# Optimization experiments

Measured on AMD Instinct MI355X. Metric: run time of the kernel, lower is better.

Reference implementation:

```python
import jax, jax.numpy as jnp
import numpy as np

T = 4096      # tokens (batch*seq)
D = 1024      # hidden_size
F = 4096      # intermediate_size
E = 8         # num_local_experts


def setup_inputs() -> dict:
    key = jax.random.key(0)
    ks = jax.random.split(key, 6)
    scale_in = 1.0 / np.sqrt(D)
    scale_f = 1.0 / np.sqrt(F)
    return {
        "x": jax.random.normal(ks[0], (T, D), jnp.float32),
        "gate_w": jax.random.normal(ks[1], (E, D), jnp.float32) * scale_in,
        "gate_b": jnp.zeros((E,), jnp.float32),
        "w1": jax.random.normal(ks[2], (E, F, D), jnp.float32) * scale_in,
        "w3": jax.random.normal(ks[3], (E, F, D), jnp.float32) * scale_in,
        "w2": jax.random.normal(ks[4], (E, D, F), jnp.float32) * scale_f,
        "top_k": 2,
    }


def reference(x, gate_w, gate_b, w1, w3, w2, top_k):
    # --- routing: gate linear -> softmax -> top-k, renormalized ---
    logits = x @ gate_w.T + gate_b                     # [T, E]
    probs = jax.nn.softmax(logits, axis=-1)            # [T, E]
    topk_p, topk_i = jax.lax.top_k(probs, top_k)       # [T, k]
    topk_p = topk_p / jnp.sum(topk_p, axis=-1, keepdims=True)
    # dense combine weights [T, E]: zeros except selected experts
    cw = jnp.zeros((x.shape[0], gate_w.shape[0]), x.dtype)
    cw = cw.at[jnp.arange(x.shape[0])[:, None], topk_i].set(topk_p)
    # --- experts: SwiGLU FFN, computed densely per expert, masked combine ---
    h1 = jnp.einsum('td,efd->etf', x, w1)              # [E, T, F]
    h3 = jnp.einsum('td,efd->etf', x, w3)              # [E, T, F]
    act = jax.nn.silu(h1) * h3                         # [E, T, F]
    expert_out = jnp.einsum('etf,edf->etd', act, w2)   # [E, T, D]
    out = jnp.einsum('etd,te->td', expert_out, cw)     # [T, D]
    return out
```

## Files before the change

kernel.cpp:

```cpp
#include <hip/hip_runtime.h>
#include <hip/hip_bf16.h>

#define T_TOK 4096
#define DIM   1024
#define FDIM  4096
#define NEXP  8
#define BM    128
#define BN    128
#define BK    32

typedef __attribute__((ext_vector_type(8))) short bf16x8_t;
typedef __attribute__((ext_vector_type(4))) float f32x4_t;

#define GLD16(gp, lp) __builtin_amdgcn_global_load_lds( \
    (const __attribute__((address_space(1))) unsigned int*)(gp), \
    (__attribute__((address_space(3))) unsigned int*)(lp), 16, 0, 0)

__device__ __forceinline__ unsigned short f2bf(float f) {
    union { __hip_bfloat16 h; unsigned short u; } c;
    c.h = __float2bfloat16(f);
    return c.u;
}
__device__ __forceinline__ uint4 pack8(const float4& a, const float4& b) {
    union { unsigned short s[8]; uint4 v; } u;
    u.s[0] = f2bf(a.x); u.s[1] = f2bf(a.y); u.s[2] = f2bf(a.z); u.s[3] = f2bf(a.w);
    u.s[4] = f2bf(b.x); u.s[5] = f2bf(b.y); u.s[6] = f2bf(b.z); u.s[7] = f2bf(b.w);
    return u.v;
}

__global__ __launch_bounds__(256) void convert_kernel(
    const float* __restrict__ src, unsigned short* __restrict__ dst, int n8)
{
    int i = blockIdx.x * 256 + threadIdx.x;
    if (i < n8) {
        const float4* s = reinterpret_cast<const float4*>(src) + (size_t)i * 2;
        float4 a = s[0], b = s[1];
        reinterpret_cast<uint4*>(dst)[i] = pack8(a, b);
    }
}

__global__ __launch_bounds__(256) void gate_kernel(
    const float* __restrict__ x, const float* __restrict__ gw,
    const float* __restrict__ gb, int* __restrict__ cnt,
    int* __restrict__ toklist, float* __restrict__ wlist)
{
    const int lane = threadIdx.x & 63;
    const int wv   = threadIdx.x >> 6;
    const int t    = blockIdx.x * 4 + wv;
    const float* xr = x + (size_t)t * DIM;

    float4 xv[4];
#pragma unroll
    for (int c = 0; c < 4; ++c)
        xv[c] = *reinterpret_cast<const float4*>(xr + c * 256 + lane * 4);

    float logit[NEXP];
#pragma unroll
    for (int e = 0; e < NEXP; ++e) {
        const float* gr = gw + e * DIM;
        float s = 0.f;
#pragma unroll
        for (int c = 0; c < 4; ++c) {
            float4 g = *reinterpret_cast<const float4*>(gr + c * 256 + lane * 4);
            s += xv[c].x * g.x + xv[c].y * g.y + xv[c].z * g.z + xv[c].w * g.w;
        }
#pragma unroll
        for (int o = 32; o > 0; o >>= 1) s += __shfl_xor(s, o, 64);
        logit[e] = s + gb[e];
    }

    if (lane == 0) {
        int i1 = 0;
#pragma unroll
        for (int e = 1; e < NEXP; ++e) if (logit[e] > logit[i1]) i1 = e;
        int i2 = (i1 == 0) ? 1 : 0;
#pragma unroll
        for (int e = 0; e < NEXP; ++e)
            if (e != i1 && e != i2 && logit[e] > logit[i2]) i2 = e;
        float eb = expf(logit[i2] - logit[i1]);
        float wA = 1.f / (1.f + eb);
        float wB = eb / (1.f + eb);
        int p = atomicAdd(&cnt[i1], 1);
        toklist[i1 * T_TOK + p] = t; wlist[i1 * T_TOK + p] = wA;
        p = atomicAdd(&cnt[i2], 1);
        toklist[i2 * T_TOK + p] = t; wlist[i2 * T_TOK + p] = wB;
    }
}

__global__ void offsets_kernel(const int* __restrict__ cnt, int* __restrict__ offs)
{
    if (threadIdx.x == 0) {
        int o = 0;
#pragma unroll
        for (int e = 0; e < NEXP; ++e) {
            offs[e] = o;
            o += ((cnt[e] + BM - 1) / BM) * BM;
        }
    }
}

__global__ __launch_bounds__(256) void gather_kernel(
    const float* __restrict__ x, const int* __restrict__ cnt,
    const int* __restrict__ offs, const int* __restrict__ toklist,
    unsigned short* __restrict__ Xp)
{
    const int b = blockIdx.x;
    const int e = b >> 12;
    const int i = b & 4095;
    const int c  = cnt[e];
    const int ca = ((c + BM - 1) >> 7) << 7;
    if (i >= ca) return;
    unsigned short* dst = Xp + (size_t)(offs[e] + i) * DIM;
    const int t4 = threadIdx.x * 4;
    ushort4 o;
    if (i < c) {
        const float* src = x + (size_t)toklist[e * T_TOK + i] * DIM;
        float4 v = *reinterpret_cast<const float4*>(src + t4);
        o.x = f2bf(v.x); o.y = f2bf(v.y); o.z = f2bf(v.z); o.w = f2bf(v.w);
    } else {
        o.x = 0; o.y = 0; o.z = 0; o.w = 0;
    }
    *reinterpret_cast<ushort4*>(dst + t4) = o;
}

__global__ __launch_bounds__(256, 2) void stageA_kernel(
    const unsigned short* __restrict__ Xp, const unsigned short* __restrict__ w1b,
    const unsigned short* __restrict__ w3b, const int* __restrict__ cnt,
    const int* __restrict__ offs, unsigned short* __restrict__ act)
{
    const int e  = blockIdx.z;
    const int c  = cnt[e];
    const int mt = blockIdx.y;
    if (mt * BM >= c) return;
    const int nt = blockIdx.x;
    const size_t slot0 = (size_t)offs[e] + (size_t)mt * BM;
    const int n0 = nt * BN;

    __shared__ __align__(16) unsigned short As[BM * BK];
    __shared__ __align__(16) unsigned short B1s[BN * BK];
    __shared__ __align__(16) unsigned short B3s[BN * BK];

    const int tid  = threadIdx.x;
    const int lane = tid & 63;
    const int wv   = tid >> 6;
    const int wm   = (wv & 1) * 64;
    const int wn   = (wv >> 1) * 64;
    const int quad = lane >> 4;
    const int r    = lane & 15;

    const int dRow = wv * 32 + (lane >> 2);
    const unsigned short* Adma  = Xp  + (slot0 + dRow) * DIM + (lane & 3) * 8;
    const unsigned short* B1dma = w1b + ((size_t)e * FDIM + n0 + dRow) * DIM + (lane & 3) * 8;
    const unsigned short* B3dma = w3b + ((size_t)e * FDIM + n0 + dRow) * DIM + (lane & 3) * 8;
    const int lds0 = (wv * 32) * BK;
    const int lds1 = (wv * 32 + 16) * BK;

    f32x4_t acc1[4][4];
    f32x4_t acc3[4][4];
#pragma unroll
    for (int i = 0; i < 4; ++i)
#pragma unroll
        for (int j = 0; j < 4; ++j) {
            acc1[i][j] = (f32x4_t){0.f, 0.f, 0.f, 0.f};
            acc3[i][j] = (f32x4_t){0.f, 0.f, 0.f, 0.f};
        }

    for (int k0 = 0; k0 < DIM; k0 += BK) {
        __syncthreads();
        GLD16(Adma + k0,             &As[lds0]);
        GLD16(Adma + k0 + 16 * DIM,  &As[lds1]);
        GLD16(B1dma + k0,            &B1s[lds0]);
        GLD16(B1dma + k0 + 16 * DIM, &B1s[lds1]);
        GLD16(B3dma + k0,            &B3s[lds0]);
        GLD16(B3dma + k0 + 16 * DIM, &B3s[lds1]);
        __syncthreads();

        bf16x8_t af[4];
#pragma unroll
        for (int i = 0; i < 4; ++i)
            af[i] = *reinterpret_cast<const bf16x8_t*>(&As[(wm + i * 16 + r) * BK + quad * 8]);
#pragma unroll
        for (int j = 0; j < 4; ++j) {
            bf16x8_t b1 = *reinterpret_cast<const bf16x8_t*>(&B1s[(wn + j * 16 + r) * BK + quad * 8]);
            bf16x8_t b3 = *reinterpret_cast<const bf16x8_t*>(&B3s[(wn + j * 16 + r) * BK + quad * 8]);
#pragma unroll
            for (int i = 0; i < 4; ++i) {
                acc1[i][j] = __builtin_amdgcn_mfma_f32_16x16x32_bf16(af[i], b1, acc1[i][j], 0, 0, 0);
                acc3[i][j] = __builtin_amdgcn_mfma_f32_16x16x32_bf16(af[i], b3, acc3[i][j], 0, 0, 0);
            }
        }
    }

    unsigned short* abase = act + slot0 * FDIM + n0;
#pragma unroll
    for (int i = 0; i < 4; ++i)
#pragma unroll
        for (int j = 0; j < 4; ++j)
#pragma unroll
            for (int rr = 0; rr < 4; ++rr) {
                int m = wm + i * 16 + quad * 4 + rr;
                int n = wn + j * 16 + r;
                float h1 = acc1[i][j][rr];
                float h3 = acc3[i][j][rr];
                float sw = h1 / (1.f + __expf(-h1)) * h3;
                abase[(size_t)m * FDIM + n] = f2bf(sw);
            }
}

__global__ __launch_bounds__(256, 3) void stageB_kernel(
    const unsigned short* __restrict__ act, const unsigned short* __restrict__ w2b,
    const int* __restrict__ cnt, const int* __restrict__ offs,
    const int* __restrict__ toklist, const float* __restrict__ wlist,
    float* __restrict__ out)
{
    const int e  = blockIdx.z & 7;
    const int ks = blockIdx.z >> 3;
    const int c  = cnt[e];
    const int mt = blockIdx.y;
    if (mt * BM >= c) return;
    const int nt = blockIdx.x;
    const size_t slot0 = (size_t)offs[e] + (size_t)mt * BM;
    const int n0 = nt * BN;
    const int kbase = ks * (FDIM / 2);

    __shared__ __align__(16) unsigned short As[BM * BK];
    __shared__ __align__(16) unsigned short Bs[BN * BK];

    const int tid  = threadIdx.x;
    const int lane = tid & 63;
    const int wv   = tid >> 6;
    const int wm   = (wv & 1) * 64;
    const int wn   = (wv >> 1) * 64;
    const int quad = lane >> 4;
    const int r    = lane & 15;

    const int dRow = wv * 32 + (lane >> 2);
    const unsigned short* Adma = act + (slot0 + dRow) * FDIM + kbase + (lane & 3) * 8;
    const unsigned short* Bdma = w2b + ((size_t)e * DIM + n0 + dRow) * FDIM + kbase + (lane & 3) * 8;
    const int lds0 = (wv * 32) * BK;
    const int lds1 = (wv * 32 + 16) * BK;

    f32x4_t acc[4][4];
#pragma unroll
    for (int i = 0; i < 4; ++i)
#pragma unroll
        for (int j = 0; j < 4; ++j) acc[i][j] = (f32x4_t){0.f, 0.f, 0.f, 0.f};

    for (int kd = 0; kd < FDIM / 2; kd += BK) {
        __syncthreads();
        GLD16(Adma + kd,             &As[lds0]);
        GLD16(Adma + kd + 16 * FDIM, &As[lds1]);
        GLD16(Bdma + kd,             &Bs[lds0]);
        GLD16(Bdma + kd + 16 * FDIM, &Bs[lds1]);
        __syncthreads();

        bf16x8_t af[4];
#pragma unroll
        for (int i = 0; i < 4; ++i)
            af[i] = *reinterpret_cast<const bf16x8_t*>(&As[(wm + i * 16 + r) * BK + quad * 8]);
#pragma unroll
        for (int j = 0; j < 4; ++j) {
            bf16x8_t bf = *reinterpret_cast<const bf16x8_t*>(&Bs[(wn + j * 16 + r) * BK + quad * 8]);
#pragma unroll
            for (int i = 0; i < 4; ++i)
                acc[i][j] = __builtin_amdgcn_mfma_f32_16x16x32_bf16(af[i], bf, acc[i][j], 0, 0, 0);
        }
    }

    const int row0 = mt * BM;
#pragma unroll
    for (int i = 0; i < 4; ++i)
#pragma unroll
        for (int rr = 0; rr < 4; ++rr) {
            int m = wm + i * 16 + quad * 4 + rr;
            int row = row0 + m;
            if (row < c) {
                int tok  = toklist[e * T_TOK + row];
                float wt = wlist[e * T_TOK + row];
                float* orow = out + (size_t)tok * DIM + n0;
#pragma unroll
                for (int j = 0; j < 4; ++j) {
                    int n = wn + j * 16 + r;
                    atomicAdd(&orow[n], wt * acc[i][j][rr]);
                }
            }
        }
}

extern "C" void kernel_launch(void* const* d_in, const int* in_sizes, int n_in,
                              void* d_out, int out_size, void* d_ws, size_t ws_size,
                              hipStream_t stream)
{
    (void)in_sizes; (void)n_in; (void)out_size; (void)ws_size;
    const float* x  = (const float*)d_in[0];
    const float* gw = (const float*)d_in[1];
    const float* gb = (const float*)d_in[2];
    const float* w1 = (const float*)d_in[3];
    const float* w3 = (const float*)d_in[4];
    const float* w2 = (const float*)d_in[5];
    float* out = (float*)d_out;

    char* ws = (char*)d_ws;
    unsigned short* Xp   = (unsigned short*)ws;
    unsigned short* act  = (unsigned short*)(ws + 18874368);
    unsigned short* w1b  = (unsigned short*)(ws + 94371840);
    unsigned short* w3b  = (unsigned short*)(ws + 161480704);
    unsigned short* w2b  = (unsigned short*)(ws + 228589568);
    int*   cnt     = (int*)(ws + 295698432);
    int*   offs    = cnt + 64;
    int*   toklist = cnt + 128;
    float* wlist   = (float*)(cnt + 128 + NEXP * T_TOK);

    hipMemsetAsync(cnt, 0, 64, stream);
    hipMemsetAsync(out, 0, (size_t)T_TOK * DIM * sizeof(float), stream);

    const int n8 = NEXP * FDIM * DIM / 8;
    convert_kernel<<<n8 / 256, 256, 0, stream>>>(w1, w1b, n8);
    convert_kernel<<<n8 / 256, 256, 0, stream>>>(w3, w3b, n8);
    convert_kernel<<<n8 / 256, 256, 0, stream>>>(w2, w2b, n8);

    gate_kernel<<<T_TOK / 4, 256, 0, stream>>>(x, gw, gb, cnt, toklist, wlist);
    offsets_kernel<<<1, 64, 0, stream>>>(cnt, offs);
    gather_kernel<<<NEXP * T_TOK, 256, 0, stream>>>(x, cnt, offs, toklist, Xp);
    stageA_kernel<<<dim3(FDIM / BN, T_TOK / BM, NEXP), 256, 0, stream>>>(Xp, w1b, w3b, cnt, offs, act);
    stageB_kernel<<<dim3(DIM / BN, T_TOK / BM, NEXP * 2), 256, 0, stream>>>(act, w2b, cnt, offs, toklist, wlist, out);
}
```

Baseline: 852.9 us.

## Pipeline stage-A GEMM with 4-deep LDS ring and fuse token gather into loads

Stage A is rewritten as a 256x128 tile kernel with 512 threads. It uses a 4-buffer LDS ring fed by global_load_lds prefetching three K-steps ahead, explicit waitcnt and barrier scheduling, s_setprio around the MFMA bursts, and an XOR-swizzled LDS layout. The separate gather kernel is removed: x is converted to bf16 once and rows are loaded indirectly through toklist, with a zero buffer standing in for padded rows. Expert offsets are now padded to 256 rows. The aim is to hide global-memory latency and drop one pass over the gathered activations. In exchange, the 128 KB LDS footprint limits how many blocks fit per CU, and the hand-tuned vmcnt counts are fragile.

```diff
diff --git a/kernel.cpp b/kernel.cpp
--- a/kernel.cpp
+++ b/kernel.cpp
@@ -8,6 +8,8 @@
 #define BM    128
 #define BN    128
 #define BK    32
+#define AM    256
+#define AK    32
 
 typedef __attribute__((ext_vector_type(8))) short bf16x8_t;
 typedef __attribute__((ext_vector_type(4))) float f32x4_t;
@@ -94,116 +96,140 @@
 #pragma unroll
         for (int e = 0; e < NEXP; ++e) {
             offs[e] = o;
-            o += ((cnt[e] + BM - 1) / BM) * BM;
-        }
-    }
-}
-
-__global__ __launch_bounds__(256) void gather_kernel(
-    const float* __restrict__ x, const int* __restrict__ cnt,
+            o += ((cnt[e] + AM - 1) / AM) * AM;
+        }
+    }
+}
+
+
+#define KSTEP(T, PF, VM)                                                       \
+  {                                                                            \
+    const int buf_ = (T) & 3;                                                  \
+    const unsigned short* Ab_  = lds + buf_ * 16384 + wm * 4096 + swz;         \
+    const unsigned short* Bb1_ = lds + buf_ * 16384 + 8192 + wnn * 1024 + swz; \
+    bf16x8_t af_[8], bf_[2];                                                   \
+    _Pragma("unroll")                                                          \
+    for (int i_ = 0; i_ < 8; ++i_)                                             \
+      af_[i_] = *reinterpret_cast<const bf16x8_t*>(Ab_ + i_ * 512);            \
+    bf_[0] = *reinterpret_cast<const bf16x8_t*>(Bb1_);                         \
+    bf_[1] = *reinterpret_cast<const bf16x8_t*>(Bb1_ + 512);                   \
+    if (PF) {                                                                  \
+      const int pb_ = ((T) + 3) & 3;                                           \
+      GLD16(Ag0 + ((T) + 3) * AK, lds + pb_ * 16384 + wv * 512);               \
+      GLD16(Ag1 + ((T) + 3) * AK, lds + pb_ * 16384 + (wv + 8) * 512);         \
+    }                                                                          \
+    __builtin_amdgcn_s_barrier();                                              \
+    asm volatile("s_waitcnt lgkmcnt(0)" ::: "memory");                         \
+    __builtin_amdgcn_sched_barrier(0);                                         \
+    __builtin_amdgcn_s_setprio(1);                                             \
+    _Pragma("unroll")                                                          \
+    for (int j_ = 0; j_ < 2; ++j_)                                             \
+      _Pragma("unroll")                                                        \
+      for (int i_ = 0; i_ < 8; ++i_)                                           \
+        acc1[i_][j_] = __builtin_amdgcn_mfma_f32_16x16x32_bf16(                \
+            af_[i_], bf_[j_], acc1[i_][j_], 0, 0, 0);                          \
+    __builtin_amdgcn_s_setprio(0);                                             \
+    __builtin_amdgcn_s_barrier();                                              \
+    bf_[0] = *reinterpret_cast<const bf16x8_t*>(Bb1_ + 4096);                  \
+    bf_[1] = *reinterpret_cast<const bf16x8_t*>(Bb1_ + 4096 + 512);            \
+    if (PF) {                                                                  \
+      const int pb_ = ((T) + 3) & 3;                                           \
+      GLD16(B1g + ((T) + 3) * AK, lds + pb_ * 16384 + 8192 + wv * 512);        \
+      GLD16(B3g + ((T) + 3) * AK, lds + pb_ * 16384 + 12288 + wv * 512);       \
+    }                                                                          \
+    asm volatile("s_waitcnt " VM ::: "memory");                                \
+    __builtin_amdgcn_s_barrier();                                              \
+    asm volatile("s_waitcnt lgkmcnt(0)" ::: "memory");                         \
+    __builtin_amdgcn_sched_barrier(0);                                         \
+    __builtin_amdgcn_s_setprio(1);                                             \
+    _Pragma("unroll")                                                          \
+    for (int j_ = 0; j_ < 2; ++j_)                                             \
+      _Pragma("unroll")                                                        \
+      for (int i_ = 0; i_ < 8; ++i_)                                           \
+        acc3[i_][j_] = __builtin_amdgcn_mfma_f32_16x16x32_bf16(                \
+            af_[i_], bf_[j_], acc3[i_][j_], 0, 0, 0);                          \
+    __builtin_amdgcn_s_setprio(0);                                             \
+    __builtin_amdgcn_s_barrier();                                              \
+  }
+
+__global__ __launch_bounds__(512, 2) void stageA_kernel(
+    const unsigned short* __restrict__ xb, const unsigned short* __restrict__ w1b,
+    const unsigned short* __restrict__ w3b, const int* __restrict__ cnt,
     const int* __restrict__ offs, const int* __restrict__ toklist,
-    unsigned short* __restrict__ Xp)
-{
-    const int b = blockIdx.x;
-    const int e = b >> 12;
-    const int i = b & 4095;
-    const int c  = cnt[e];
-    const int ca = ((c + BM - 1) >> 7) << 7;
-    if (i >= ca) return;
-    unsigned short* dst = Xp + (size_t)(offs[e] + i) * DIM;
-    const int t4 = threadIdx.x * 4;
-    ushort4 o;
-    if (i < c) {
-        const float* src = x + (size_t)toklist[e * T_TOK + i] * DIM;
-        float4 v = *reinterpret_cast<const float4*>(src + t4);
-        o.x = f2bf(v.x); o.y = f2bf(v.y); o.z = f2bf(v.z); o.w = f2bf(v.w);
-    } else {
-        o.x = 0; o.y = 0; o.z = 0; o.w = 0;
-    }
-    *reinterpret_cast<ushort4*>(dst + t4) = o;
-}
-
-__global__ __launch_bounds__(256, 2) void stageA_kernel(
-    const unsigned short* __restrict__ Xp, const unsigned short* __restrict__ w1b,
-    const unsigned short* __restrict__ w3b, const int* __restrict__ cnt,
-    const int* __restrict__ offs, unsigned short* __restrict__ act)
+    const unsigned short* __restrict__ zbuf, unsigned short* __restrict__ act)
 {
     const int e  = blockIdx.z;
     const int c  = cnt[e];
     const int mt = blockIdx.y;
-    if (mt * BM >= c) return;
+    if (mt * AM >= c) return;
     const int nt = blockIdx.x;
-    const size_t slot0 = (size_t)offs[e] + (size_t)mt * BM;
-    const int n0 = nt * BN;
-
-    __shared__ __align__(16) unsigned short As[BM * BK];
-    __shared__ __align__(16) unsigned short B1s[BN * BK];
-    __shared__ __align__(16) unsigned short B3s[BN * BK];
+    const int n0 = nt * 128;
+
+    __shared__ __align__(16) unsigned short lds[4 * 16384];
 
     const int tid  = threadIdx.x;
     const int lane = tid & 63;
     const int wv   = tid >> 6;
-    const int wm   = (wv & 1) * 64;
-    const int wn   = (wv >> 1) * 64;
+    const int wm   = wv >> 2;
+    const int wnn  = wv & 3;
     const int quad = lane >> 4;
     const int r    = lane & 15;
 
-    const int dRow = wv * 32 + (lane >> 2);
-    const unsigned short* Adma  = Xp  + (slot0 + dRow) * DIM + (lane & 3) * 8;
-    const unsigned short* B1dma = w1b + ((size_t)e * FDIM + n0 + dRow) * DIM + (lane & 3) * 8;
-    const unsigned short* B3dma = w3b + ((size_t)e * FDIM + n0 + dRow) * DIM + (lane & 3) * 8;
-    const int lds0 = (wv * 32) * BK;
-    const int lds1 = (wv * 32 + 16) * BK;
-
-    f32x4_t acc1[4][4];
-    f32x4_t acc3[4][4];
-#pragma unroll
-    for (int i = 0; i < 4; ++i)
-#pragma unroll
-        for (int j = 0; j < 4; ++j) {
+    const int swz = (r * 32 + quad * 8) ^ (((r >> 1) & 3) << 3);
+
+    const int wr = (lane >> 2) & 15;
+    const int wc = (((lane ^ (lane >> 3)) & 1) << 3) |
+                   ((((lane >> 1) ^ (lane >> 4)) & 1) << 4);
+
+    const int stRow = wv * 16 + wr;
+    const int ar0 = mt * AM + stRow;
+    const int ar1 = ar0 + 128;
+    const unsigned short* Ag0 = (ar0 < c)
+        ? xb + (size_t)toklist[e * T_TOK + ar0] * DIM + wc : zbuf + wc;
+    const unsigned short* Ag1 = (ar1 < c)
+        ? xb + (size_t)toklist[e * T_TOK + ar1] * DIM + wc : zbuf + wc;
+    const unsigned short* B1g = w1b + ((size_t)e * FDIM + n0 + stRow) * DIM + wc;
+    const unsigned short* B3g = w3b + ((size_t)e * FDIM + n0 + stRow) * DIM + wc;
+
+    f32x4_t acc1[8][2], acc3[8][2];
+#pragma unroll
+    for (int i = 0; i < 8; ++i)
+#pragma unroll
+        for (int j = 0; j < 2; ++j) {
             acc1[i][j] = (f32x4_t){0.f, 0.f, 0.f, 0.f};
             acc3[i][j] = (f32x4_t){0.f, 0.f, 0.f, 0.f};
         }
 
-    for (int k0 = 0; k0 < DIM; k0 += BK) {
-        __syncthreads();
-        GLD16(Adma + k0,             &As[lds0]);
-        GLD16(Adma + k0 + 16 * DIM,  &As[lds1]);
-        GLD16(B1dma + k0,            &B1s[lds0]);
-        GLD16(B1dma + k0 + 16 * DIM, &B1s[lds1]);
-        GLD16(B3dma + k0,            &B3s[lds0]);
-        GLD16(B3dma + k0 + 16 * DIM, &B3s[lds1]);
-        __syncthreads();
-
-        bf16x8_t af[4];
-#pragma unroll
-        for (int i = 0; i < 4; ++i)
-            af[i] = *reinterpret_cast<const bf16x8_t*>(&As[(wm + i * 16 + r) * BK + quad * 8]);
-#pragma unroll
-        for (int j = 0; j < 4; ++j) {
-            bf16x8_t b1 = *reinterpret_cast<const bf16x8_t*>(&B1s[(wn + j * 16 + r) * BK + quad * 8]);
-            bf16x8_t b3 = *reinterpret_cast<const bf16x8_t*>(&B3s[(wn + j * 16 + r) * BK + quad * 8]);
-#pragma unroll
-            for (int i = 0; i < 4; ++i) {
-                acc1[i][j] = __builtin_amdgcn_mfma_f32_16x16x32_bf16(af[i], b1, acc1[i][j], 0, 0, 0);
-                acc3[i][j] = __builtin_amdgcn_mfma_f32_16x16x32_bf16(af[i], b3, acc3[i][j], 0, 0, 0);
-            }
-        }
-    }
-
-    unsigned short* abase = act + slot0 * FDIM + n0;
-#pragma unroll
-    for (int i = 0; i < 4; ++i)
-#pragma unroll
-        for (int j = 0; j < 4; ++j)
+#pragma unroll
+    for (int t = 0; t < 3; ++t) {
+        GLD16(Ag0 + t * AK, lds + t * 16384 + wv * 512);
+        GLD16(Ag1 + t * AK, lds + t * 16384 + (wv + 8) * 512);
+        GLD16(B1g + t * AK, lds + t * 16384 + 8192 + wv * 512);
+        GLD16(B3g + t * AK, lds + t * 16384 + 12288 + wv * 512);
+    }
+    asm volatile("s_waitcnt vmcnt(8)" ::: "memory");
+    __builtin_amdgcn_s_barrier();
+
+#pragma unroll 1
+    for (int t = 0; t < 28; ++t) KSTEP(t, 1, "vmcnt(8)");
+    KSTEP(28, 1, "vmcnt(8)");
+    KSTEP(29, 0, "vmcnt(4)");
+    KSTEP(30, 0, "vmcnt(0)");
+    KSTEP(31, 0, "vmcnt(0)");
+
+    const size_t slot0 = (size_t)offs[e] + (size_t)mt * AM;
+    unsigned short* abase = act + (slot0 + wm * 128 + quad * 4) * (size_t)FDIM
+                          + n0 + wnn * 32 + r;
+#pragma unroll
+    for (int i = 0; i < 8; ++i)
+#pragma unroll
+        for (int j = 0; j < 2; ++j)
 #pragma unroll
             for (int rr = 0; rr < 4; ++rr) {
-                int m = wm + i * 16 + quad * 4 + rr;
-                int n = wn + j * 16 + r;
                 float h1 = acc1[i][j][rr];
                 float h3 = acc3[i][j][rr];
                 float sw = h1 / (1.f + __expf(-h1)) * h3;
-                abase[(size_t)m * FDIM + n] = f2bf(sw);
+                abase[(size_t)(i * 16 + rr) * FDIM + j * 16] = f2bf(sw);
             }
 }
 
@@ -301,27 +327,31 @@
     float* out = (float*)d_out;
 
     char* ws = (char*)d_ws;
-    unsigned short* Xp   = (unsigned short*)ws;
-    unsigned short* act  = (unsigned short*)(ws + 18874368);
-    unsigned short* w1b  = (unsigned short*)(ws + 94371840);
-    unsigned short* w3b  = (unsigned short*)(ws + 161480704);
-    unsigned short* w2b  = (unsigned short*)(ws + 228589568);
-    int*   cnt     = (int*)(ws + 295698432);
+    unsigned short* xb   = (unsigned short*)ws;
+    unsigned short* act  = (unsigned short*)(ws + 8388608);
+    unsigned short* w1b  = (unsigned short*)(ws + 92274688);
+    unsigned short* w3b  = (unsigned short*)(ws + 159383552);
+    unsigned short* w2b  = (unsigned short*)(ws + 226492416);
+    unsigned short* zbuf = (unsigned short*)(ws + 293601280);
+    int*   cnt     = (int*)(ws + 293605376);
     int*   offs    = cnt + 64;
     int*   toklist = cnt + 128;
     float* wlist   = (float*)(cnt + 128 + NEXP * T_TOK);
 
     hipMemsetAsync(cnt, 0, 64, stream);
+    hipMemsetAsync(zbuf, 0, 4096, stream);
     hipMemsetAsync(out, 0, (size_t)T_TOK * DIM * sizeof(float), stream);
 
     const int n8 = NEXP * FDIM * DIM / 8;
     convert_kernel<<<n8 / 256, 256, 0, stream>>>(w1, w1b, n8);
     convert_kernel<<<n8 / 256, 256, 0, stream>>>(w3, w3b, n8);
     convert_kernel<<<n8 / 256, 256, 0, stream>>>(w2, w2b, n8);
+    convert_kernel<<<(T_TOK * DIM / 8) / 256, 256, 0, stream>>>(x, xb, T_TOK * DIM / 8);
 
     gate_kernel<<<T_TOK / 4, 256, 0, stream>>>(x, gw, gb, cnt, toklist, wlist);
     offsets_kernel<<<1, 64, 0, stream>>>(cnt, offs);
-    gather_kernel<<<NEXP * T_TOK, 256, 0, stream>>>(x, cnt, offs, toklist, Xp);
-    stageA_kernel<<<dim3(FDIM / BN, T_TOK / BM, NEXP), 256, 0, stream>>>(Xp, w1b, w3b, cnt, offs, act);
-    stageB_kernel<<<dim3(DIM / BN, T_TOK / BM, NEXP * 2), 256, 0, stream>>>(act, w2b, cnt, offs, toklist, wlist, out);
-}
+    stageA_kernel<<<dim3(FDIM / 128, T_TOK / AM, NEXP), 512, 0, stream>>>(
+        xb, w1b, w3b, cnt, offs, toklist, zbuf, act);
+    stageB_kernel<<<dim3(DIM / BN, T_TOK / BM, NEXP * 2), 256, 0, stream>>>(
+        act, w2b, cnt, offs, toklist, wlist, out);
+}
```

Result: faster. 825.5 us (-3.2%).
